# Kernel tuning notes

Hardware: AMD Instinct MI355X
Metric: run time of the kernel (lower is better)

## Reference

```python
import jax, jax.numpy as jnp
import numpy as np
import math

D, DF, H, L, V, T_MAX = 768, 3072, 12, 4, 32000, 2048
HD = D // H
B, T = 2, 2048


def setup_inputs() -> dict:
    key = jax.random.key(0)
    ks = jax.random.split(key, 20)
    s = 0.02
    inp = {
        'ids': jax.random.randint(ks[0], (B, T), 0, V),
        'te': jax.random.normal(ks[1], (V, D), jnp.float32) * s,  # tied with head
        'pe': jax.random.normal(ks[2], (T_MAX, D), jnp.float32) * s,
        'ln1_s': jnp.ones((L, D), jnp.float32),
        'ln1_b': jnp.zeros((L, D), jnp.float32),
        'qkv_w': jax.random.normal(ks[3], (L, D, 3 * H * HD), jnp.float32) * s,
        'qkv_b': jnp.zeros((L, 3 * H * HD), jnp.float32),
        'out_w': jax.random.normal(ks[4], (L, H * HD, D), jnp.float32) * s,
        'out_b': jnp.zeros((L, D), jnp.float32),
        'ln2_s': jnp.ones((L, D), jnp.float32),
        'ln2_b': jnp.zeros((L, D), jnp.float32),
        'up_w': jax.random.normal(ks[5], (L, D, DF), jnp.float32) * s,
        'up_b': jnp.zeros((L, DF), jnp.float32),
        'dn_w': jax.random.normal(ks[6], (L, DF, D), jnp.float32) * s,
        'dn_b': jnp.zeros((L, D), jnp.float32),
        'lnf_s': jnp.ones((D,), jnp.float32),
        'lnf_b': jnp.zeros((D,), jnp.float32),
    }
    return inp


def _layernorm(x, s, b, eps=1e-5):
    mu = jnp.mean(x, axis=-1, keepdims=True)
    var = jnp.mean(jnp.square(x - mu), axis=-1, keepdims=True)
    return (x - mu) * jax.lax.rsqrt(var + eps) * s + b


def reference(ids, te, pe, ln1_s, ln1_b, qkv_w, qkv_b, out_w, out_b,
              ln2_s, ln2_b, up_w, up_b, dn_w, dn_b, lnf_s, lnf_b):
    b, t = ids.shape
    x = te[ids] + pe[jnp.arange(t)][None, :, :]  # [b,t,d]
    causal = jnp.tril(jnp.ones((t, t), bool))[None, None]  # [1,1,t,t]
    neg = jnp.asarray(-jnp.inf, x.dtype)
    for i in range(L):
        h = _layernorm(x, ln1_s[i], ln1_b[i])
        qkv = (h @ qkv_w[i] + qkv_b[i]).reshape(b, t, 3, H, HD)
        q, k, v = [jnp.moveaxis(qkv[:, :, j], 1, 2) for j in range(3)]  # [b,h,t,hd]
        sc = jnp.einsum('bhqd,bhkd->bhqk', q, k) / math.sqrt(HD)
        sc = jnp.where(causal, sc, neg)
        a = jax.nn.softmax(sc, axis=-1)
        o = jnp.einsum('bhqk,bhkd->bhqd', a, v)
        o = jnp.moveaxis(o, 1, 2).reshape(b, t, H * HD)
        x = x + o @ out_w[i] + out_b[i]
        h = _layernorm(x, ln2_s[i], ln2_b[i])
        x = x + jax.nn.silu(h @ up_w[i] + up_b[i]) @ dn_w[i] + dn_b[i]
    logits = _layernorm(x, lnf_s, lnf_b) @ te.T  # tied head, no bias
    return logits
```

## Files before the change

### kernel.cpp

```cpp
#include <hip/hip_runtime.h>

typedef unsigned short u16;

#define TSEQ 2048
#define DMODEL 768
#define DFF 3072
#define NHEAD 12
#define HDIM 64
#define NLAYER 4
#define NVOCAB 32000
#define MROWS 4096

typedef __attribute__((ext_vector_type(8))) __bf16 bf16x8;
typedef __attribute__((ext_vector_type(4))) float f32x4;
typedef __attribute__((ext_vector_type(8))) unsigned short us8;

__device__ __forceinline__ float u2f(u16 u) {
  return __uint_as_float(((unsigned int)u) << 16);
}
__device__ __forceinline__ u16 f2bu(float f) {
  unsigned int u = __float_as_uint(f);
  u += 0x7fffu + ((u >> 16) & 1u);
  return (u16)(u >> 16);
}
__device__ __forceinline__ int probe_f32(const void* probe) {
  return ((const u16*)probe)[0] == 0 ? 1 : 0;
}
__device__ __forceinline__ float ldf(const void* p, size_t i, int f32) {
  return f32 ? ((const float*)p)[i] : u2f(((const u16*)p)[i]);
}
__device__ __forceinline__ void ld8(const void* p, size_t i, int f32, float* o) {
  if (f32) {
    const float* q = (const float*)p + i;
    float4 a = *(const float4*)q, b = *(const float4*)(q + 4);
    o[0]=a.x; o[1]=a.y; o[2]=a.z; o[3]=a.w; o[4]=b.x; o[5]=b.y; o[6]=b.z; o[7]=b.w;
  } else {
    const u16* q = (const u16*)p + i;
    ushort4 a = *(const ushort4*)q, b = *(const ushort4*)(q + 4);
    o[0]=u2f(a.x); o[1]=u2f(a.y); o[2]=u2f(a.z); o[3]=u2f(a.w);
    o[4]=u2f(b.x); o[5]=u2f(b.y); o[6]=u2f(b.z); o[7]=u2f(b.w);
  }
}
__device__ __forceinline__ us8 pack8(const float* f) {
  us8 r;
#pragma unroll
  for (int i = 0; i < 8; i++) r[i] = f2bu(f[i]);
  return r;
}
__device__ __forceinline__ void gld16(const u16* g, u16* l) {
  __builtin_amdgcn_global_load_lds(
      (const __attribute__((address_space(1))) void*)g,
      (__attribute__((address_space(3))) void*)l, 16, 0, 0);
}

__global__ __launch_bounds__(256) void embed_kernel(const int* __restrict__ ids,
    const void* __restrict__ te, const void* __restrict__ pe, float* __restrict__ x,
    const void* probe) {
  int f32 = probe_f32(probe);
  int m = blockIdx.x;
  int t = m & (TSEQ - 1);
  int id = ids[m];
  float* xr = x + (size_t)m * DMODEL;
  for (int d = threadIdx.x; d < DMODEL; d += 256)
    xr[d] = ldf(te, (size_t)id * DMODEL + d, f32) + ldf(pe, (size_t)t * DMODEL + d, f32);
}

__global__ __launch_bounds__(256) void ln_kernel(const float* __restrict__ x,
    const void* __restrict__ s, const void* __restrict__ b, long soff,
    u16* __restrict__ h, const void* probe) {
  int f32 = probe_f32(probe);
  int m = blockIdx.x;
  const float* xr = x + (size_t)m * DMODEL;
  float v[3];
  float lsum = 0.f, lsq = 0.f;
#pragma unroll
  for (int j = 0; j < 3; j++) {
    float t = xr[threadIdx.x + j * 256];
    v[j] = t; lsum += t; lsq += t * t;
  }
#pragma unroll
  for (int off = 32; off > 0; off >>= 1) {
    lsum += __shfl_down(lsum, off);
    lsq  += __shfl_down(lsq, off);
  }
  __shared__ float wsum[4], wsq[4];
  __shared__ float mu_s, rs_s;
  int wid = threadIdx.x >> 6, lane = threadIdx.x & 63;
  if (lane == 0) { wsum[wid] = lsum; wsq[wid] = lsq; }
  __syncthreads();
  if (threadIdx.x == 0) {
    float su = wsum[0] + wsum[1] + wsum[2] + wsum[3];
    float sq = wsq[0] + wsq[1] + wsq[2] + wsq[3];
    float mu = su * (1.f / DMODEL);
    float var = sq * (1.f / DMODEL) - mu * mu;
    mu_s = mu;
    rs_s = rsqrtf(var + 1e-5f);
  }
  __syncthreads();
  float mu = mu_s, rs = rs_s;
  u16* hr = h + (size_t)m * DMODEL;
#pragma unroll
  for (int j = 0; j < 3; j++) {
    int d = threadIdx.x + j * 256;
    hr[d] = f2bu((v[j] - mu) * rs * ldf(s, soff + d, f32) + ldf(b, soff + d, f32));
  }
}

__global__ __launch_bounds__(256) void wtrans_kernel(const void* __restrict__ W,
    u16* __restrict__ Wt, int K, int N, const void* probe) {
  const int f32 = probe_f32(probe);
  __shared__ u16 t[64][33];
  const size_t ls = (size_t)K * N;
  const size_t off = (size_t)blockIdx.z * ls;
  const int k0 = blockIdx.y << 6, n0 = blockIdx.x << 5;
  const int tid = threadIdx.x;
  const int tn = tid & 31, tk8 = tid >> 5;
#pragma unroll
  for (int p = 0; p < 8; p++) {
    int k = (p << 3) + tk8;
    t[k][tn] = f2bu(ldf(W, off + (size_t)(k0 + k) * N + n0 + tn, f32));
  }
  __syncthreads();
  const int kp = (tid & 31) << 1, nb = tid >> 5;
#pragma unroll
  for (int p = 0; p < 4; p++) {
    int n = (p << 3) + nb;
    ushort2 v; v.x = t[kp][n]; v.y = t[kp + 1][n];
    *(ushort2*)&Wt[off + (size_t)(n0 + n) * K + k0 + kp] = v;
  }
}

__global__ __launch_bounds__(256) void cvt_bf16_kernel(const void* __restrict__ src,
    u16* __restrict__ dst, size_t n, const void* probe) {
  const int f32 = probe_f32(probe);
  size_t i = ((size_t)blockIdx.x * 256 + threadIdx.x) * 8;
  if (i >= n) return;
  float v[8];
  ld8(src, i, f32, v);
  *(us8*)&dst[i] = pack8(v);
}

__global__ __launch_bounds__(256) void gemm_mfma(const u16* __restrict__ A,
    const u16* __restrict__ Wt, long woff, const void* __restrict__ bias, long boff,
    const float* resid, void* C, int N, int K, int mode, const void* probe) {
  const int f32 = probe_f32(probe);
  __shared__ __align__(16) u16 As[128 * 32];
  __shared__ __align__(16) u16 Bs[128 * 32];
  const int tid = threadIdx.x;
  const int m0 = blockIdx.y << 7, n0 = blockIdx.x << 7;
  const int lane = tid & 63;
  const int w = tid >> 6;
  const int wr = ((tid >> 7) & 1) << 6;
  const int wc = ((tid >> 6) & 1) << 6;
  const int fm = lane & 15;
  const int kl = lane >> 4;
  const int srow = (w << 4) + (lane >> 2);
  const int skc  = (lane & 3) << 3;

  f32x4 acc[4][4];
#pragma unroll
  for (int i = 0; i < 4; i++)
#pragma unroll
    for (int j = 0; j < 4; j++) acc[i][j] = (f32x4){0.f, 0.f, 0.f, 0.f};

  const u16* Ab = A + (size_t)(m0 + srow) * K + skc;
  const u16* Wb = Wt + (size_t)woff + (size_t)(n0 + srow) * K + skc;
  const size_t rstep = (size_t)64 * K;
  u16* lA0 = As + (w << 9);
  u16* lA1 = As + ((w + 4) << 9);
  u16* lB0 = Bs + (w << 9);
  u16* lB1 = Bs + ((w + 4) << 9);

  for (int k0 = 0; k0 < K; k0 += 32) {
    gld16(Ab + k0, lA0);
    gld16(Ab + rstep + k0, lA1);
    gld16(Wb + k0, lB0);
    gld16(Wb + rstep + k0, lB1);
    __syncthreads();
    bf16x8 af[4], bfr[4];
#pragma unroll
    for (int i = 0; i < 4; i++)
      af[i] = *reinterpret_cast<const bf16x8*>(&As[((wr + i * 16 + fm) << 5) + (kl << 3)]);
#pragma unroll
    for (int j = 0; j < 4; j++)
      bfr[j] = *reinterpret_cast<const bf16x8*>(&Bs[((wc + j * 16 + fm) << 5) + (kl << 3)]);
#pragma unroll
    for (int i = 0; i < 4; i++)
#pragma unroll
      for (int j = 0; j < 4; j++)
        acc[i][j] = __builtin_amdgcn_mfma_f32_16x16x32_bf16(af[i], bfr[j], acc[i][j], 0, 0, 0);
    __syncthreads();
  }

  const int rb = m0 + wr + (kl << 2);
  const int cb = n0 + wc + fm;
  float bv[4];
#pragma unroll
  for (int j = 0; j < 4; j++) bv[j] = ldf(bias, boff + cb + j * 16, f32);
#pragma unroll
  for (int i = 0; i < 4; i++) {
#pragma unroll
    for (int e = 0; e < 4; e++) {
      size_t roff = (size_t)(rb + i * 16 + e) * N;
#pragma unroll
      for (int j = 0; j < 4; j++) {
        float v = acc[i][j][e] + bv[j];
        if (mode == 1) {
          ((float*)C)[roff + cb + j * 16] = v + resid[roff + cb + j * 16];
        } else {
          if (mode == 2) v = v / (1.f + __expf(-v));
          ((u16*)C)[roff + cb + j * 16] = f2bu(v);
        }
      }
    }
  }
}

__global__ __launch_bounds__(256) void gemm_head_mfma(const u16* __restrict__ A,
    const u16* __restrict__ Wtb, void* __restrict__ C, const void* probe) {
  const int f32 = probe_f32(probe);
  __shared__ __align__(16) u16 As[128 * 32];
  __shared__ __align__(16) u16 Bs[128 * 32];
  const int tid = threadIdx.x;
  const int m0 = blockIdx.x << 7, n0 = blockIdx.y << 7;
  const int lane = tid & 63;
  const int w = tid >> 6;
  const int wr = ((tid >> 7) & 1) << 6;
  const int wc = ((tid >> 6) & 1) << 6;
  const int fm = lane & 15;
  const int kl = lane >> 4;
  const int srow = (w << 4) + (lane >> 2);
  const int skc  = (lane & 3) << 3;

  f32x4 acc[4][4];
#pragma unroll
  for (int i = 0; i < 4; i++)
#pragma unroll
    for (int j = 0; j < 4; j++) acc[i][j] = (f32x4){0.f, 0.f, 0.f, 0.f};

  const u16* Ab = A + (size_t)(m0 + srow) * DMODEL + skc;
  const u16* Wb = Wtb + (size_t)(n0 + srow) * DMODEL + skc;
  const size_t rstep = (size_t)64 * DMODEL;
  u16* lA0 = As + (w << 9);
  u16* lA1 = As + ((w + 4) << 9);
  u16* lB0 = Bs + (w << 9);
  u16* lB1 = Bs + ((w + 4) << 9);

  for (int k0 = 0; k0 < DMODEL; k0 += 32) {
    gld16(Ab + k0, lA0);
    gld16(Ab + rstep + k0, lA1);
    gld16(Wb + k0, lB0);
    gld16(Wb + rstep + k0, lB1);
    __syncthreads();
    bf16x8 af[4], bfr[4];
#pragma unroll
    for (int i = 0; i < 4; i++)
      af[i] = *reinterpret_cast<const bf16x8*>(&As[((wr + i * 16 + fm) << 5) + (kl << 3)]);
#pragma unroll
    for (int j = 0; j < 4; j++)
      bfr[j] = *reinterpret_cast<const bf16x8*>(&Bs[((wc + j * 16 + fm) << 5) + (kl << 3)]);
#pragma unroll
    for (int i = 0; i < 4; i++)
#pragma unroll
      for (int j = 0; j < 4; j++)
        acc[i][j] = __builtin_amdgcn_mfma_f32_16x16x32_bf16(af[i], bfr[j], acc[i][j], 0, 0, 0);
    __syncthreads();
  }

  const int rbase = m0 + wr + (kl << 2);
  const int cbase = n0 + wc + fm;
#pragma unroll
  for (int i = 0; i < 4; i++) {
#pragma unroll
    for (int j = 0; j < 4; j++) {
#pragma unroll
      for (int e = 0; e < 4; e++) {
        size_t off = (size_t)(rbase + i * 16 + e) * NVOCAB + cbase + j * 16;
        if (f32) ((float*)C)[off] = acc[i][j][e];
        else     ((u16*)C)[off]   = f2bu(acc[i][j][e]);
      }
    }
  }
}

__global__ __launch_bounds__(256) void attn_mfma(const u16* __restrict__ qkv,
                                                 u16* __restrict__ o) {
  const int qt = blockIdx.x, hh = blockIdx.y, bb = blockIdx.z;
  __shared__ __align__(16) u16 Ks[64][72];
  __shared__ __align__(16) u16 Vt[64][72];
  __shared__ __align__(16) u16 Ps[64][72];
  const int tid = threadIdx.x;
  const int w = tid >> 6, lane = tid & 63;
  const int fm = lane & 15, kl = lane >> 4;

  bf16x8 aq[2];
  {
    const u16* qrow = qkv + ((size_t)(bb * TSEQ + qt * 64 + w * 16 + fm)) * 2304 + hh * 64;
#pragma unroll
    for (int c = 0; c < 2; c++) {
      us8 u = *(const us8*)(qrow + c * 32 + kl * 8);
      aq[c] = *(bf16x8*)&u;
    }
  }

  float m_r[4], l_r[4];
#pragma unroll
  for (int e = 0; e < 4; e++) { m_r[e] = -3e38f; l_r[e] = 0.f; }
  f32x4 oacc[4];
#pragma unroll
  for (int j = 0; j < 4; j++) oacc[j] = (f32x4){0.f, 0.f, 0.f, 0.f};

  for (int kt = 0; kt <= qt; kt++) {
    const size_t kbase = ((size_t)(bb * TSEQ + kt * 64)) * 2304 + hh * 64;
#pragma unroll
    for (int it = 0; it < 2; it++) {
      int idx = tid + it * 256;
      int row = idx >> 3, cb = (idx & 7) << 3;
      *(us8*)&Ks[row][cb] = *(const us8*)(qkv + kbase + (size_t)row * 2304 + 768 + cb);
      int row2 = idx & 63, cb2 = (idx >> 6) << 3;
      us8 vv = *(const us8*)(qkv + kbase + (size_t)row2 * 2304 + 1536 + cb2);
#pragma unroll
      for (int e = 0; e < 8; e++) Vt[cb2 + e][row2] = vv[e];
    }
    __syncthreads();

    f32x4 sacc[4];
#pragma unroll
    for (int j = 0; j < 4; j++) sacc[j] = (f32x4){0.f, 0.f, 0.f, 0.f};
#pragma unroll
    for (int ck = 0; ck < 2; ck++) {
      bf16x8 kb[4];
#pragma unroll
      for (int j = 0; j < 4; j++)
        kb[j] = *reinterpret_cast<const bf16x8*>(&Ks[j * 16 + fm][ck * 32 + (kl << 3)]);
#pragma unroll
      for (int j = 0; j < 4; j++)
        sacc[j] = __builtin_amdgcn_mfma_f32_16x16x32_bf16(aq[ck], kb[j], sacc[j], 0, 0, 0);
    }
#pragma unroll
    for (int j = 0; j < 4; j++)
#pragma unroll
      for (int e = 0; e < 4; e++) sacc[j][e] *= 0.125f;
    if (kt == qt) {
      const int qrow0 = w * 16 + (kl << 2);
#pragma unroll
      for (int j = 0; j < 4; j++)
#pragma unroll
        for (int e = 0; e < 4; e++)
          if (j * 16 + fm > qrow0 + e) sacc[j][e] = -3e38f;
    }
    float pmax[4];
#pragma unroll
    for (int e = 0; e < 4; e++) {
      pmax[e] = fmaxf(fmaxf(sacc[0][e], sacc[1][e]), fmaxf(sacc[2][e], sacc[3][e]));
    }
#pragma unroll
    for (int msk = 1; msk < 16; msk <<= 1)
#pragma unroll
      for (int e = 0; e < 4; e++) pmax[e] = fmaxf(pmax[e], __shfl_xor(pmax[e], msk));
    float al[4];
#pragma unroll
    for (int e = 0; e < 4; e++) {
      float nm = fmaxf(m_r[e], pmax[e]);
      al[e] = __expf(m_r[e] - nm);
      m_r[e] = nm;
    }
    float psum[4] = {0.f, 0.f, 0.f, 0.f};
#pragma unroll
    for (int j = 0; j < 4; j++)
#pragma unroll
      for (int e = 0; e < 4; e++) {
        float p = __expf(sacc[j][e] - m_r[e]);
        sacc[j][e] = p;
        psum[e] += p;
      }
#pragma unroll
    for (int j = 0; j < 4; j++)
#pragma unroll
      for (int e = 0; e < 4; e++)
        Ps[w * 16 + (kl << 2) + e][j * 16 + fm] = f2bu(sacc[j][e]);
#pragma unroll
    for (int msk = 1; msk < 16; msk <<= 1)
#pragma unroll
      for (int e = 0; e < 4; e++) psum[e] += __shfl_xor(psum[e], msk);
#pragma unroll
    for (int e = 0; e < 4; e++) l_r[e] = l_r[e] * al[e] + psum[e];
#pragma unroll
    for (int j = 0; j < 4; j++)
#pragma unroll
      for (int e = 0; e < 4; e++) oacc[j][e] *= al[e];
#pragma unroll
    for (int ck = 0; ck < 2; ck++) {
      bf16x8 pa = *reinterpret_cast<const bf16x8*>(&Ps[w * 16 + fm][ck * 32 + (kl << 3)]);
      bf16x8 vb[4];
#pragma unroll
      for (int j = 0; j < 4; j++)
        vb[j] = *reinterpret_cast<const bf16x8*>(&Vt[j * 16 + fm][ck * 32 + (kl << 3)]);
#pragma unroll
      for (int j = 0; j < 4; j++)
        oacc[j] = __builtin_amdgcn_mfma_f32_16x16x32_bf16(pa, vb[j], oacc[j], 0, 0, 0);
    }
    __syncthreads();
  }

  float linv[4];
#pragma unroll
  for (int e = 0; e < 4; e++) linv[e] = 1.f / l_r[e];
#pragma unroll
  for (int e = 0; e < 4; e++) {
    size_t ob = ((size_t)(bb * TSEQ + qt * 64 + w * 16 + (kl << 2) + e)) * DMODEL + hh * 64 + fm;
#pragma unroll
    for (int j = 0; j < 4; j++) o[ob + j * 16] = f2bu(oacc[j][e] * linv[e]);
  }
}

extern "C" void kernel_launch(void* const* d_in, const int* in_sizes, int n_in,
                              void* d_out, int out_size, void* d_ws, size_t ws_size,
                              hipStream_t stream) {
  const int* ids = (const int*)d_in[0];
  const void* te    = d_in[1];
  const void* pe    = d_in[2];
  const void* ln1_s = d_in[3];
  const void* ln1_b = d_in[4];
  const void* qkv_w = d_in[5];
  const void* qkv_b = d_in[6];
  const void* out_w = d_in[7];
  const void* out_b = d_in[8];
  const void* ln2_s = d_in[9];
  const void* ln2_b = d_in[10];
  const void* up_w  = d_in[11];
  const void* up_b  = d_in[12];
  const void* dn_w  = d_in[13];
  const void* dn_b  = d_in[14];
  const void* lnf_s = d_in[15];
  const void* lnf_b = d_in[16];
  const void* probe = ln1_s;

  float* x  = (float*)d_ws;
  u16* h    = (u16*)(x + (size_t)MROWS * DMODEL);
  u16* ob   = h + (size_t)MROWS * DMODEL;
  u16* qu   = ob + (size_t)MROWS * DMODEL;
  u16* wt   = qu + (size_t)MROWS * DFF;
  const size_t qkv_t_sz = (size_t)2304 * 768;
  const size_t out_t_sz = (size_t)768 * 768;
  const size_t up_t_sz  = (size_t)3072 * 768;
  const size_t dn_t_sz  = (size_t)768 * 3072;
  u16* qkv_t = wt;
  u16* out_t = qkv_t + NLAYER * qkv_t_sz;
  u16* up_t  = out_t + NLAYER * out_t_sz;
  u16* dn_t  = up_t  + NLAYER * up_t_sz;
  u16* tebf  = dn_t + NLAYER * dn_t_sz;
  const size_t te_sz = (size_t)NVOCAB * DMODEL;

  embed_kernel<<<MROWS, 256, 0, stream>>>(ids, te, pe, x, probe);

  wtrans_kernel<<<dim3(2304/32, 768/64, NLAYER), 256, 0, stream>>>(qkv_w, qkv_t, 768, 2304, probe);
  wtrans_kernel<<<dim3(768/32,  768/64, NLAYER), 256, 0, stream>>>(out_w, out_t, 768, 768, probe);
  wtrans_kernel<<<dim3(3072/32, 768/64, NLAYER), 256, 0, stream>>>(up_w,  up_t,  768, 3072, probe);
  wtrans_kernel<<<dim3(768/32, 3072/64, NLAYER), 256, 0, stream>>>(dn_w,  dn_t,  3072, 768, probe);
  cvt_bf16_kernel<<<(int)((te_sz / 8 + 255) / 256), 256, 0, stream>>>(te, tebf, te_sz, probe);

  for (int l = 0; l < NLAYER; l++) {
    long lD = (long)l * DMODEL;
    ln_kernel<<<MROWS, 256, 0, stream>>>(x, ln1_s, ln1_b, lD, h, probe);
    gemm_mfma<<<dim3(18, 32), 256, 0, stream>>>(h, qkv_t, (long)l * qkv_t_sz,
        qkv_b, (long)l * 2304, nullptr, qu, 2304, DMODEL, 0, probe);
    attn_mfma<<<dim3(32, 12, 2), 256, 0, stream>>>(qu, ob);
    gemm_mfma<<<dim3(6, 32), 256, 0, stream>>>(ob, out_t, (long)l * out_t_sz,
        out_b, lD, x, x, DMODEL, DMODEL, 1, probe);
    ln_kernel<<<MROWS, 256, 0, stream>>>(x, ln2_s, ln2_b, lD, h, probe);
    gemm_mfma<<<dim3(24, 32), 256, 0, stream>>>(h, up_t, (long)l * up_t_sz,
        up_b, (long)l * DFF, nullptr, qu, DFF, DMODEL, 2, probe);
    gemm_mfma<<<dim3(6, 32), 256, 0, stream>>>(qu, dn_t, (long)l * dn_t_sz,
        dn_b, lD, x, x, DMODEL, DFF, 1, probe);
  }
  ln_kernel<<<MROWS, 256, 0, stream>>>(x, lnf_s, lnf_b, 0, h, probe);
  gemm_head_mfma<<<dim3(32, 250), 256, 0, stream>>>(h, tebf, d_out, probe);
}
```

Before: 2.302 ms.

## Enlarge attention query tile to 128 rows with register-prefetched K/V and reversed scheduling

The attention kernel now processes 128 query rows per block, with each wave handling two 16-row groups, so every K/V tile loaded into shared memory is reused across twice as many queries. The next K/V tile is prefetched into registers while the current tile is computed. Blocks are launched in reverse order so the heaviest causal tiles start first. In exchange, register pressure rises, the grid shrinks to half as many blocks, and waves whose rows are fully masked sit idle on the last tile.

Measured after the change: 2.377 ms. 1.03x slower.

```diff
diff --git a/kernel.cpp b/kernel.cpp
--- a/kernel.cpp
+++ b/kernel.cpp
@@ -285,132 +285,182 @@
 
 __global__ __launch_bounds__(256) void attn_mfma(const u16* __restrict__ qkv,
                                                  u16* __restrict__ o) {
-  const int qt = blockIdx.x, hh = blockIdx.y, bb = blockIdx.z;
+  const int qb = gridDim.x - 1 - blockIdx.x;
+  const int hh = blockIdx.y, bb = blockIdx.z;
   __shared__ __align__(16) u16 Ks[64][72];
   __shared__ __align__(16) u16 Vt[64][72];
-  __shared__ __align__(16) u16 Ps[64][72];
+  __shared__ __align__(16) u16 Ps[128][72];
   const int tid = threadIdx.x;
   const int w = tid >> 6, lane = tid & 63;
   const int fm = lane & 15, kl = lane >> 4;
 
-  bf16x8 aq[2];
-  {
-    const u16* qrow = qkv + ((size_t)(bb * TSEQ + qt * 64 + w * 16 + fm)) * 2304 + hh * 64;
+  const int krow0 = tid >> 3, kcb0 = (tid & 7) << 3;
+  const int krow1 = (tid + 256) >> 3, kcb1 = ((tid + 256) & 7) << 3;
+  const int vrow0 = tid & 63, vcb0 = (tid >> 6) << 3;
+  const int vcb1 = vcb0 + 32;
+
+  bf16x8 aq[2][2];
+#pragma unroll
+  for (int g = 0; g < 2; g++) {
+    const u16* qrow = qkv + ((size_t)(bb * TSEQ + qb * 128 + w * 32 + g * 16 + fm)) * 2304 + hh * 64;
 #pragma unroll
     for (int c = 0; c < 2; c++) {
       us8 u = *(const us8*)(qrow + c * 32 + kl * 8);
-      aq[c] = *(bf16x8*)&u;
-    }
-  }
-
-  float m_r[4], l_r[4];
-#pragma unroll
-  for (int e = 0; e < 4; e++) { m_r[e] = -3e38f; l_r[e] = 0.f; }
-  f32x4 oacc[4];
-#pragma unroll
-  for (int j = 0; j < 4; j++) oacc[j] = (f32x4){0.f, 0.f, 0.f, 0.f};
-
-  for (int kt = 0; kt <= qt; kt++) {
-    const size_t kbase = ((size_t)(bb * TSEQ + kt * 64)) * 2304 + hh * 64;
-#pragma unroll
-    for (int it = 0; it < 2; it++) {
-      int idx = tid + it * 256;
-      int row = idx >> 3, cb = (idx & 7) << 3;
-      *(us8*)&Ks[row][cb] = *(const us8*)(qkv + kbase + (size_t)row * 2304 + 768 + cb);
-      int row2 = idx & 63, cb2 = (idx >> 6) << 3;
-      us8 vv = *(const us8*)(qkv + kbase + (size_t)row2 * 2304 + 1536 + cb2);
-#pragma unroll
-      for (int e = 0; e < 8; e++) Vt[cb2 + e][row2] = vv[e];
+      aq[g][c] = *(bf16x8*)&u;
+    }
+  }
+
+  float m_r[2][4], l_r[2][4];
+#pragma unroll
+  for (int g = 0; g < 2; g++)
+#pragma unroll
+    for (int e = 0; e < 4; e++) { m_r[g][e] = -3e38f; l_r[g][e] = 0.f; }
+  f32x4 oacc[2][4];
+#pragma unroll
+  for (int g = 0; g < 2; g++)
+#pragma unroll
+    for (int j = 0; j < 4; j++) oacc[g][j] = (f32x4){0.f, 0.f, 0.f, 0.f};
+
+  const int ktop  = 2 * qb + 1;
+  const int kmaxw = 2 * qb + (w >> 1);
+
+  {
+    const size_t kb0 = ((size_t)(bb * TSEQ)) * 2304 + hh * 64;
+    *(us8*)&Ks[krow0][kcb0] = *(const us8*)(qkv + kb0 + (size_t)krow0 * 2304 + 768 + kcb0);
+    *(us8*)&Ks[krow1][kcb1] = *(const us8*)(qkv + kb0 + (size_t)krow1 * 2304 + 768 + kcb1);
+    us8 v0 = *(const us8*)(qkv + kb0 + (size_t)vrow0 * 2304 + 1536 + vcb0);
+    us8 v1 = *(const us8*)(qkv + kb0 + (size_t)vrow0 * 2304 + 1536 + vcb1);
+#pragma unroll
+    for (int e = 0; e < 8; e++) { Vt[vcb0 + e][vrow0] = v0[e]; Vt[vcb1 + e][vrow0] = v1[e]; }
+  }
+  __syncthreads();
+
+  for (int kt = 0; kt <= ktop; kt++) {
+    const int active = (kt <= kmaxw);
+    f32x4 sacc[2][4];
+#pragma unroll
+    for (int g = 0; g < 2; g++)
+#pragma unroll
+      for (int j = 0; j < 4; j++) sacc[g][j] = (f32x4){0.f, 0.f, 0.f, 0.f};
+    if (active) {
+#pragma unroll
+      for (int ck = 0; ck < 2; ck++) {
+        bf16x8 kb[4];
+#pragma unroll
+        for (int j = 0; j < 4; j++)
+          kb[j] = *reinterpret_cast<const bf16x8*>(&Ks[j * 16 + fm][ck * 32 + (kl << 3)]);
+#pragma unroll
+        for (int g = 0; g < 2; g++)
+#pragma unroll
+          for (int j = 0; j < 4; j++)
+            sacc[g][j] = __builtin_amdgcn_mfma_f32_16x16x32_bf16(aq[g][ck], kb[j], sacc[g][j], 0, 0, 0);
+      }
+    }
+    us8 kpre0, kpre1, vpre0, vpre1;
+    const int nkt = kt + 1;
+    if (nkt <= ktop) {
+      const size_t kbn = ((size_t)(bb * TSEQ + nkt * 64)) * 2304 + hh * 64;
+      kpre0 = *(const us8*)(qkv + kbn + (size_t)krow0 * 2304 + 768 + kcb0);
+      kpre1 = *(const us8*)(qkv + kbn + (size_t)krow1 * 2304 + 768 + kcb1);
+      vpre0 = *(const us8*)(qkv + kbn + (size_t)vrow0 * 2304 + 1536 + vcb0);
+      vpre1 = *(const us8*)(qkv + kbn + (size_t)vrow0 * 2304 + 1536 + vcb1);
+    }
+    if (active) {
+#pragma unroll
+      for (int g = 0; g < 2; g++)
+#pragma unroll
+        for (int j = 0; j < 4; j++)
+#pragma unroll
+          for (int e = 0; e < 4; e++) sacc[g][j][e] *= 0.125f;
+      if (kt == kmaxw) {
+#pragma unroll
+        for (int g = 0; g < 2; g++) {
+          const int qg = qb * 128 + w * 32 + g * 16 + (kl << 2);
+#pragma unroll
+          for (int j = 0; j < 4; j++)
+#pragma unroll
+            for (int e = 0; e < 4; e++)
+              if (kt * 64 + j * 16 + fm > qg + e) sacc[g][j][e] = -3e38f;
+        }
+      }
+#pragma unroll
+      for (int g = 0; g < 2; g++) {
+        float pmax[4];
+#pragma unroll
+        for (int e = 0; e < 4; e++)
+          pmax[e] = fmaxf(fmaxf(sacc[g][0][e], sacc[g][1][e]), fmaxf(sacc[g][2][e], sacc[g][3][e]));
+#pragma unroll
+        for (int msk = 1; msk < 16; msk <<= 1)
+#pragma unroll
+          for (int e = 0; e < 4; e++) pmax[e] = fmaxf(pmax[e], __shfl_xor(pmax[e], msk));
+        float al[4];
+#pragma unroll
+        for (int e = 0; e < 4; e++) {
+          float nm = fmaxf(m_r[g][e], pmax[e]);
+          al[e] = __expf(m_r[g][e] - nm);
+          m_r[g][e] = nm;
+        }
+        float psum[4] = {0.f, 0.f, 0.f, 0.f};
+#pragma unroll
+        for (int j = 0; j < 4; j++)
+#pragma unroll
+          for (int e = 0; e < 4; e++) {
+            float p = __expf(sacc[g][j][e] - m_r[g][e]);
+            sacc[g][j][e] = p;
+            psum[e] += p;
+          }
+#pragma unroll
+        for (int j = 0; j < 4; j++)
+#pragma unroll
+          for (int e = 0; e < 4; e++)
+            Ps[w * 32 + g * 16 + (kl << 2) + e][j * 16 + fm] = f2bu(sacc[g][j][e]);
+#pragma unroll
+        for (int msk = 1; msk < 16; msk <<= 1)
+#pragma unroll
+          for (int e = 0; e < 4; e++) psum[e] += __shfl_xor(psum[e], msk);
+#pragma unroll
+        for (int e = 0; e < 4; e++) l_r[g][e] = l_r[g][e] * al[e] + psum[e];
+#pragma unroll
+        for (int j = 0; j < 4; j++)
+#pragma unroll
+          for (int e = 0; e < 4; e++) oacc[g][j][e] *= al[e];
+      }
+#pragma unroll
+      for (int ck = 0; ck < 2; ck++) {
+        bf16x8 vb[4];
+#pragma unroll
+        for (int j = 0; j < 4; j++)
+          vb[j] = *reinterpret_cast<const bf16x8*>(&Vt[j * 16 + fm][ck * 32 + (kl << 3)]);
+#pragma unroll
+        for (int g = 0; g < 2; g++) {
+          bf16x8 pa = *reinterpret_cast<const bf16x8*>(&Ps[w * 32 + g * 16 + fm][ck * 32 + (kl << 3)]);
+#pragma unroll
+          for (int j = 0; j < 4; j++)
+            oacc[g][j] = __builtin_amdgcn_mfma_f32_16x16x32_bf16(pa, vb[j], oacc[g][j], 0, 0, 0);
+        }
+      }
     }
     __syncthreads();
-
-    f32x4 sacc[4];
-#pragma unroll
-    for (int j = 0; j < 4; j++) sacc[j] = (f32x4){0.f, 0.f, 0.f, 0.f};
-#pragma unroll
-    for (int ck = 0; ck < 2; ck++) {
-      bf16x8 kb[4];
-#pragma unroll
-      for (int j = 0; j < 4; j++)
-        kb[j] = *reinterpret_cast<const bf16x8*>(&Ks[j * 16 + fm][ck * 32 + (kl << 3)]);
-#pragma unroll
-      for (int j = 0; j < 4; j++)
-        sacc[j] = __builtin_amdgcn_mfma_f32_16x16x32_bf16(aq[ck], kb[j], sacc[j], 0, 0, 0);
-    }
-#pragma unroll
-    for (int j = 0; j < 4; j++)
-#pragma unroll
-      for (int e = 0; e < 4; e++) sacc[j][e] *= 0.125f;
-    if (kt == qt) {
-      const int qrow0 = w * 16 + (kl << 2);
-#pragma unroll
-      for (int j = 0; j < 4; j++)
-#pragma unroll
-        for (int e = 0; e < 4; e++)
-          if (j * 16 + fm > qrow0 + e) sacc[j][e] = -3e38f;
-    }
-    float pmax[4];
+    if (nkt <= ktop) {
+      *(us8*)&Ks[krow0][kcb0] = kpre0;
+      *(us8*)&Ks[krow1][kcb1] = kpre1;
+#pragma unroll
+      for (int e = 0; e < 8; e++) { Vt[vcb0 + e][vrow0] = vpre0[e]; Vt[vcb1 + e][vrow0] = vpre1[e]; }
+    }
+    __syncthreads();
+  }
+
+#pragma unroll
+  for (int g = 0; g < 2; g++) {
+    float linv[4];
+#pragma unroll
+    for (int e = 0; e < 4; e++) linv[e] = 1.f / l_r[g][e];
 #pragma unroll
     for (int e = 0; e < 4; e++) {
-      pmax[e] = fmaxf(fmaxf(sacc[0][e], sacc[1][e]), fmaxf(sacc[2][e], sacc[3][e]));
-    }
-#pragma unroll
-    for (int msk = 1; msk < 16; msk <<= 1)
-#pragma unroll
-      for (int e = 0; e < 4; e++) pmax[e] = fmaxf(pmax[e], __shfl_xor(pmax[e], msk));
-    float al[4];
-#pragma unroll
-    for (int e = 0; e < 4; e++) {
-      float nm = fmaxf(m_r[e], pmax[e]);
-      al[e] = __expf(m_r[e] - nm);
-      m_r[e] = nm;
-    }
-    float psum[4] = {0.f, 0.f, 0.f, 0.f};
-#pragma unroll
-    for (int j = 0; j < 4; j++)
-#pragma unroll
-      for (int e = 0; e < 4; e++) {
-        float p = __expf(sacc[j][e] - m_r[e]);
-        sacc[j][e] = p;
-        psum[e] += p;
-      }
-#pragma unroll
-    for (int j = 0; j < 4; j++)
-#pragma unroll
-      for (int e = 0; e < 4; e++)
-        Ps[w * 16 + (kl << 2) + e][j * 16 + fm] = f2bu(sacc[j][e]);
-#pragma unroll
-    for (int msk = 1; msk < 16; msk <<= 1)
-#pragma unroll
-      for (int e = 0; e < 4; e++) psum[e] += __shfl_xor(psum[e], msk);
-#pragma unroll
-    for (int e = 0; e < 4; e++) l_r[e] = l_r[e] * al[e] + psum[e];
-#pragma unroll
-    for (int j = 0; j < 4; j++)
-#pragma unroll
-      for (int e = 0; e < 4; e++) oacc[j][e] *= al[e];
-#pragma unroll
-    for (int ck = 0; ck < 2; ck++) {
-      bf16x8 pa = *reinterpret_cast<const bf16x8*>(&Ps[w * 16 + fm][ck * 32 + (kl << 3)]);
-      bf16x8 vb[4];
-#pragma unroll
-      for (int j = 0; j < 4; j++)
-        vb[j] = *reinterpret_cast<const bf16x8*>(&Vt[j * 16 + fm][ck * 32 + (kl << 3)]);
-#pragma unroll
-      for (int j = 0; j < 4; j++)
-        oacc[j] = __builtin_amdgcn_mfma_f32_16x16x32_bf16(pa, vb[j], oacc[j], 0, 0, 0);
-    }
-    __syncthreads();
-  }
-
-  float linv[4];
-#pragma unroll
-  for (int e = 0; e < 4; e++) linv[e] = 1.f / l_r[e];
-#pragma unroll
-  for (int e = 0; e < 4; e++) {
-    size_t ob = ((size_t)(bb * TSEQ + qt * 64 + w * 16 + (kl << 2) + e)) * DMODEL + hh * 64 + fm;
-#pragma unroll
-    for (int j = 0; j < 4; j++) o[ob + j * 16] = f2bu(oacc[j][e] * linv[e]);
+      size_t ob = ((size_t)(bb * TSEQ + qb * 128 + w * 32 + g * 16 + (kl << 2) + e)) * DMODEL + hh * 64 + fm;
+#pragma unroll
+      for (int j = 0; j < 4; j++) o[ob + j * 16] = f2bu(oacc[g][j][e] * linv[e]);
+    }
   }
 }
 
@@ -465,7 +515,7 @@
     ln_kernel<<<MROWS, 256, 0, stream>>>(x, ln1_s, ln1_b, lD, h, probe);
     gemm_mfma<<<dim3(18, 32), 256, 0, stream>>>(h, qkv_t, (long)l * qkv_t_sz,
         qkv_b, (long)l * 2304, nullptr, qu, 2304, DMODEL, 0, probe);
-    attn_mfma<<<dim3(32, 12, 2), 256, 0, stream>>>(qu, ob);
+    attn_mfma<<<dim3(16, 12, 2), 256, 0, stream>>>(qu, ob);
     gemm_mfma<<<dim3(6, 32), 256, 0, stream>>>(ob, out_t, (long)l * out_t_sz,
         out_b, lD, x, x, DMODEL, DMODEL, 1, probe);
     ln_kernel<<<MROWS, 256, 0, stream>>>(x, ln2_s, ln2_b, lD, h, probe);
```

## Enlarge attention query tile to 128 with register-prefetched K/V and reversed block order

Applied to the files above, without the earlier changes.

The attention kernel now uses 512 threads per block covering 128 query rows, so each K/V tile loaded into shared memory serves twice as many queries. The next K/V tile is fetched into registers while the current tile is being computed, then written to LDS after a barrier, which overlaps global load latency with MFMA and softmax work. Blocks are launched in reverse order so the longest causal rows start first, improving load balance. The cost is wasted iterations for the lower-half waves on the last tile, larger blocks, and an extra barrier per iteration.

After: 2.357 ms. 1.02x slower.

```diff
diff --git a/kernel.cpp b/kernel.cpp
--- a/kernel.cpp
+++ b/kernel.cpp
@@ -283,19 +283,23 @@
   }
 }
 
-__global__ __launch_bounds__(256) void attn_mfma(const u16* __restrict__ qkv,
+__global__ __launch_bounds__(512) void attn_mfma(const u16* __restrict__ qkv,
                                                  u16* __restrict__ o) {
-  const int qt = blockIdx.x, hh = blockIdx.y, bb = blockIdx.z;
+  const int qb = gridDim.x - 1 - blockIdx.x;
+  const int hh = blockIdx.y, bb = blockIdx.z;
   __shared__ __align__(16) u16 Ks[64][72];
   __shared__ __align__(16) u16 Vt[64][72];
-  __shared__ __align__(16) u16 Ps[64][72];
+  __shared__ __align__(16) u16 Ps[128][72];
   const int tid = threadIdx.x;
   const int w = tid >> 6, lane = tid & 63;
   const int fm = lane & 15, kl = lane >> 4;
 
+  const int krow = tid >> 3, kcb = (tid & 7) << 3;
+  const int vrow = tid & 63, vcb = (tid >> 6) << 3;
+
   bf16x8 aq[2];
   {
-    const u16* qrow = qkv + ((size_t)(bb * TSEQ + qt * 64 + w * 16 + fm)) * 2304 + hh * 64;
+    const u16* qrow = qkv + ((size_t)(bb * TSEQ + qb * 128 + w * 16 + fm)) * 2304 + hh * 64;
 #pragma unroll
     for (int c = 0; c < 2; c++) {
       us8 u = *(const us8*)(qrow + c * 32 + kl * 8);
@@ -310,95 +314,111 @@
 #pragma unroll
   for (int j = 0; j < 4; j++) oacc[j] = (f32x4){0.f, 0.f, 0.f, 0.f};
 
-  for (int kt = 0; kt <= qt; kt++) {
-    const size_t kbase = ((size_t)(bb * TSEQ + kt * 64)) * 2304 + hh * 64;
-#pragma unroll
-    for (int it = 0; it < 2; it++) {
-      int idx = tid + it * 256;
-      int row = idx >> 3, cb = (idx & 7) << 3;
-      *(us8*)&Ks[row][cb] = *(const us8*)(qkv + kbase + (size_t)row * 2304 + 768 + cb);
-      int row2 = idx & 63, cb2 = (idx >> 6) << 3;
-      us8 vv = *(const us8*)(qkv + kbase + (size_t)row2 * 2304 + 1536 + cb2);
-#pragma unroll
-      for (int e = 0; e < 8; e++) Vt[cb2 + e][row2] = vv[e];
-    }
-    __syncthreads();
-
+  const int ktop  = 2 * qb + 1;
+  const int kmaxw = 2 * qb + (w >> 2);
+
+  {
+    const size_t kb0 = ((size_t)(bb * TSEQ)) * 2304 + hh * 64;
+    *(us8*)&Ks[krow][kcb] = *(const us8*)(qkv + kb0 + (size_t)krow * 2304 + 768 + kcb);
+    us8 v0 = *(const us8*)(qkv + kb0 + (size_t)vrow * 2304 + 1536 + vcb);
+#pragma unroll
+    for (int e = 0; e < 8; e++) Vt[vcb + e][vrow] = v0[e];
+  }
+  __syncthreads();
+
+  for (int kt = 0; kt <= ktop; kt++) {
+    const int active = (kt <= kmaxw);
     f32x4 sacc[4];
 #pragma unroll
     for (int j = 0; j < 4; j++) sacc[j] = (f32x4){0.f, 0.f, 0.f, 0.f};
-#pragma unroll
-    for (int ck = 0; ck < 2; ck++) {
-      bf16x8 kb[4];
-#pragma unroll
-      for (int j = 0; j < 4; j++)
-        kb[j] = *reinterpret_cast<const bf16x8*>(&Ks[j * 16 + fm][ck * 32 + (kl << 3)]);
-#pragma unroll
-      for (int j = 0; j < 4; j++)
-        sacc[j] = __builtin_amdgcn_mfma_f32_16x16x32_bf16(aq[ck], kb[j], sacc[j], 0, 0, 0);
-    }
-#pragma unroll
-    for (int j = 0; j < 4; j++)
-#pragma unroll
-      for (int e = 0; e < 4; e++) sacc[j][e] *= 0.125f;
-    if (kt == qt) {
-      const int qrow0 = w * 16 + (kl << 2);
+    if (active) {
+#pragma unroll
+      for (int ck = 0; ck < 2; ck++) {
+        bf16x8 kb[4];
+#pragma unroll
+        for (int j = 0; j < 4; j++)
+          kb[j] = *reinterpret_cast<const bf16x8*>(&Ks[j * 16 + fm][ck * 32 + (kl << 3)]);
+#pragma unroll
+        for (int j = 0; j < 4; j++)
+          sacc[j] = __builtin_amdgcn_mfma_f32_16x16x32_bf16(aq[ck], kb[j], sacc[j], 0, 0, 0);
+      }
+    }
+    us8 kpre, vpre;
+    const int nkt = kt + 1;
+    if (nkt <= ktop) {
+      const size_t kbn = ((size_t)(bb * TSEQ + nkt * 64)) * 2304 + hh * 64;
+      kpre = *(const us8*)(qkv + kbn + (size_t)krow * 2304 + 768 + kcb);
+      vpre = *(const us8*)(qkv + kbn + (size_t)vrow * 2304 + 1536 + vcb);
+    }
+    if (active) {
+#pragma unroll
+      for (int j = 0; j < 4; j++)
+#pragma unroll
+        for (int e = 0; e < 4; e++) sacc[j][e] *= 0.125f;
+      if (kt == kmaxw) {
+        const int qg = qb * 128 + w * 16 + (kl << 2);
+#pragma unroll
+        for (int j = 0; j < 4; j++)
+#pragma unroll
+          for (int e = 0; e < 4; e++)
+            if (kt * 64 + j * 16 + fm > qg + e) sacc[j][e] = -3e38f;
+      }
+      float pmax[4];
+#pragma unroll
+      for (int e = 0; e < 4; e++)
+        pmax[e] = fmaxf(fmaxf(sacc[0][e], sacc[1][e]), fmaxf(sacc[2][e], sacc[3][e]));
+#pragma unroll
+      for (int msk = 1; msk < 16; msk <<= 1)
+#pragma unroll
+        for (int e = 0; e < 4; e++) pmax[e] = fmaxf(pmax[e], __shfl_xor(pmax[e], msk));
+      float al[4];
+#pragma unroll
+      for (int e = 0; e < 4; e++) {
+        float nm = fmaxf(m_r[e], pmax[e]);
+        al[e] = __expf(m_r[e] - nm);
+        m_r[e] = nm;
+      }
+      float psum[4] = {0.f, 0.f, 0.f, 0.f};
+#pragma unroll
+      for (int j = 0; j < 4; j++)
+#pragma unroll
+        for (int e = 0; e < 4; e++) {
+          float p = __expf(sacc[j][e] - m_r[e]);
+          sacc[j][e] = p;
+          psum[e] += p;
+        }
 #pragma unroll
       for (int j = 0; j < 4; j++)
 #pragma unroll
         for (int e = 0; e < 4; e++)
-          if (j * 16 + fm > qrow0 + e) sacc[j][e] = -3e38f;
-    }
-    float pmax[4];
-#pragma unroll
-    for (int e = 0; e < 4; e++) {
-      pmax[e] = fmaxf(fmaxf(sacc[0][e], sacc[1][e]), fmaxf(sacc[2][e], sacc[3][e]));
-    }
-#pragma unroll
-    for (int msk = 1; msk < 16; msk <<= 1)
-#pragma unroll
-      for (int e = 0; e < 4; e++) pmax[e] = fmaxf(pmax[e], __shfl_xor(pmax[e], msk));
-    float al[4];
-#pragma unroll
-    for (int e = 0; e < 4; e++) {
-      float nm = fmaxf(m_r[e], pmax[e]);
-      al[e] = __expf(m_r[e] - nm);
-      m_r[e] = nm;
-    }
-    float psum[4] = {0.f, 0.f, 0.f, 0.f};
-#pragma unroll
-    for (int j = 0; j < 4; j++)
-#pragma unroll
-      for (int e = 0; e < 4; e++) {
-        float p = __expf(sacc[j][e] - m_r[e]);
-        sacc[j][e] = p;
-        psum[e] += p;
-      }
-#pragma unroll
-    for (int j = 0; j < 4; j++)
-#pragma unroll
-      for (int e = 0; e < 4; e++)
-        Ps[w * 16 + (kl << 2) + e][j * 16 + fm] = f2bu(sacc[j][e]);
-#pragma unroll
-    for (int msk = 1; msk < 16; msk <<= 1)
-#pragma unroll
-      for (int e = 0; e < 4; e++) psum[e] += __shfl_xor(psum[e], msk);
-#pragma unroll
-    for (int e = 0; e < 4; e++) l_r[e] = l_r[e] * al[e] + psum[e];
-#pragma unroll
-    for (int j = 0; j < 4; j++)
-#pragma unroll
-      for (int e = 0; e < 4; e++) oacc[j][e] *= al[e];
-#pragma unroll
-    for (int ck = 0; ck < 2; ck++) {
-      bf16x8 pa = *reinterpret_cast<const bf16x8*>(&Ps[w * 16 + fm][ck * 32 + (kl << 3)]);
-      bf16x8 vb[4];
-#pragma unroll
-      for (int j = 0; j < 4; j++)
-        vb[j] = *reinterpret_cast<const bf16x8*>(&Vt[j * 16 + fm][ck * 32 + (kl << 3)]);
-#pragma unroll
-      for (int j = 0; j < 4; j++)
-        oacc[j] = __builtin_amdgcn_mfma_f32_16x16x32_bf16(pa, vb[j], oacc[j], 0, 0, 0);
+          Ps[w * 16 + (kl << 2) + e][j * 16 + fm] = f2bu(sacc[j][e]);
+#pragma unroll
+      for (int msk = 1; msk < 16; msk <<= 1)
+#pragma unroll
+        for (int e = 0; e < 4; e++) psum[e] += __shfl_xor(psum[e], msk);
+#pragma unroll
+      for (int e = 0; e < 4; e++) l_r[e] = l_r[e] * al[e] + psum[e];
+#pragma unroll
+      for (int j = 0; j < 4; j++)
+#pragma unroll
+        for (int e = 0; e < 4; e++) oacc[j][e] *= al[e];
+#pragma unroll
+      for (int ck = 0; ck < 2; ck++) {
+        bf16x8 pa = *reinterpret_cast<const bf16x8*>(&Ps[w * 16 + fm][ck * 32 + (kl << 3)]);
+        bf16x8 vb[4];
+#pragma unroll
+        for (int j = 0; j < 4; j++)
+          vb[j] = *reinterpret_cast<const bf16x8*>(&Vt[j * 16 + fm][ck * 32 + (kl << 3)]);
+#pragma unroll
+        for (int j = 0; j < 4; j++)
+          oacc[j] = __builtin_amdgcn_mfma_f32_16x16x32_bf16(pa, vb[j], oacc[j], 0, 0, 0);
+      }
+    }
+    __syncthreads();
+    if (nkt <= ktop) {
+      *(us8*)&Ks[krow][kcb] = kpre;
+#pragma unroll
+      for (int e = 0; e < 8; e++) Vt[vcb + e][vrow] = vpre[e];
     }
     __syncthreads();
   }
@@ -408,7 +428,7 @@
   for (int e = 0; e < 4; e++) linv[e] = 1.f / l_r[e];
 #pragma unroll
   for (int e = 0; e < 4; e++) {
-    size_t ob = ((size_t)(bb * TSEQ + qt * 64 + w * 16 + (kl << 2) + e)) * DMODEL + hh * 64 + fm;
+    size_t ob = ((size_t)(bb * TSEQ + qb * 128 + w * 16 + (kl << 2) + e)) * DMODEL + hh * 64 + fm;
 #pragma unroll
     for (int j = 0; j < 4; j++) o[ob + j * 16] = f2bu(oacc[j][e] * linv[e]);
   }
@@ -465,7 +485,7 @@
     ln_kernel<<<MROWS, 256, 0, stream>>>(x, ln1_s, ln1_b, lD, h, probe);
     gemm_mfma<<<dim3(18, 32), 256, 0, stream>>>(h, qkv_t, (long)l * qkv_t_sz,
         qkv_b, (long)l * 2304, nullptr, qu, 2304, DMODEL, 0, probe);
-    attn_mfma<<<dim3(32, 12, 2), 256, 0, stream>>>(qu, ob);
+    attn_mfma<<<dim3(16, 12, 2), 512, 0, stream>>>(qu, ob);
     gemm_mfma<<<dim3(6, 32), 256, 0, stream>>>(ob, out_t, (long)l * out_t_sz,
         out_b, lD, x, x, DMODEL, DMODEL, 1, probe);
     ln_kernel<<<MROWS, 256, 0, stream>>>(x, ln2_s, ln2_b, lD, h, probe);
```

## Prefetch K/V into registers in attention, reverse tile order, widen head GEMM K-tile

Applied to the files above, without the earlier changes.

The attention kernel now starts the global loads for the next K/V tile into registers while the current tile is being computed, then writes them to shared memory after a barrier. This overlaps load latency with compute at the cost of more registers and an extra barrier per iteration. Query blocks are also scheduled in reverse, so the longest causal rows launch first and load balancing improves. Separately, the tied-head GEMM now uses a K-tile of 64 instead of 32, which halves the number of barriers and loop iterations but doubles the shared memory per block.

New measurement: 2.271 ms. About the same (-1.4%).

```diff
diff --git a/kernel.cpp b/kernel.cpp
--- a/kernel.cpp
+++ b/kernel.cpp
@@ -219,8 +219,8 @@
 __global__ __launch_bounds__(256) void gemm_head_mfma(const u16* __restrict__ A,
     const u16* __restrict__ Wtb, void* __restrict__ C, const void* probe) {
   const int f32 = probe_f32(probe);
-  __shared__ __align__(16) u16 As[128 * 32];
-  __shared__ __align__(16) u16 Bs[128 * 32];
+  __shared__ __align__(16) u16 As[128 * 64];
+  __shared__ __align__(16) u16 Bs[128 * 64];
   const int tid = threadIdx.x;
   const int m0 = blockIdx.x << 7, n0 = blockIdx.y << 7;
   const int lane = tid & 63;
@@ -229,8 +229,8 @@
   const int wc = ((tid >> 6) & 1) << 6;
   const int fm = lane & 15;
   const int kl = lane >> 4;
-  const int srow = (w << 4) + (lane >> 2);
-  const int skc  = (lane & 3) << 3;
+  const int srow = (w << 5) + (lane >> 3);
+  const int skc  = (lane & 7) << 3;
 
   f32x4 acc[4][4];
 #pragma unroll
@@ -240,30 +240,31 @@
 
   const u16* Ab = A + (size_t)(m0 + srow) * DMODEL + skc;
   const u16* Wb = Wtb + (size_t)(n0 + srow) * DMODEL + skc;
-  const size_t rstep = (size_t)64 * DMODEL;
-  u16* lA0 = As + (w << 9);
-  u16* lA1 = As + ((w + 4) << 9);
-  u16* lB0 = Bs + (w << 9);
-  u16* lB1 = Bs + ((w + 4) << 9);
-
-  for (int k0 = 0; k0 < DMODEL; k0 += 32) {
-    gld16(Ab + k0, lA0);
-    gld16(Ab + rstep + k0, lA1);
-    gld16(Wb + k0, lB0);
-    gld16(Wb + rstep + k0, lB1);
-    __syncthreads();
-    bf16x8 af[4], bfr[4];
-#pragma unroll
-    for (int i = 0; i < 4; i++)
-      af[i] = *reinterpret_cast<const bf16x8*>(&As[((wr + i * 16 + fm) << 5) + (kl << 3)]);
-#pragma unroll
-    for (int j = 0; j < 4; j++)
-      bfr[j] = *reinterpret_cast<const bf16x8*>(&Bs[((wc + j * 16 + fm) << 5) + (kl << 3)]);
-#pragma unroll
-    for (int i = 0; i < 4; i++)
-#pragma unroll
-      for (int j = 0; j < 4; j++)
-        acc[i][j] = __builtin_amdgcn_mfma_f32_16x16x32_bf16(af[i], bfr[j], acc[i][j], 0, 0, 0);
+  u16* lA = As + (w << 11);
+  u16* lB = Bs + (w << 11);
+
+  for (int k0 = 0; k0 < DMODEL; k0 += 64) {
+#pragma unroll
+    for (int i = 0; i < 4; i++) {
+      gld16(Ab + (size_t)(8 * i) * DMODEL + k0, lA + (i << 9));
+      gld16(Wb + (size_t)(8 * i) * DMODEL + k0, lB + (i << 9));
+    }
+    __syncthreads();
+#pragma unroll
+    for (int kh = 0; kh < 2; kh++) {
+      bf16x8 af[4], bfr[4];
+#pragma unroll
+      for (int i = 0; i < 4; i++)
+        af[i] = *reinterpret_cast<const bf16x8*>(&As[((wr + i * 16 + fm) << 6) + (kh << 5) + (kl << 3)]);
+#pragma unroll
+      for (int j = 0; j < 4; j++)
+        bfr[j] = *reinterpret_cast<const bf16x8*>(&Bs[((wc + j * 16 + fm) << 6) + (kh << 5) + (kl << 3)]);
+#pragma unroll
+      for (int i = 0; i < 4; i++)
+#pragma unroll
+        for (int j = 0; j < 4; j++)
+          acc[i][j] = __builtin_amdgcn_mfma_f32_16x16x32_bf16(af[i], bfr[j], acc[i][j], 0, 0, 0);
+    }
     __syncthreads();
   }
 
@@ -285,7 +286,8 @@
 
 __global__ __launch_bounds__(256) void attn_mfma(const u16* __restrict__ qkv,
                                                  u16* __restrict__ o) {
-  const int qt = blockIdx.x, hh = blockIdx.y, bb = blockIdx.z;
+  const int qb = gridDim.x - 1 - blockIdx.x;
+  const int hh = blockIdx.y, bb = blockIdx.z;
   __shared__ __align__(16) u16 Ks[64][72];
   __shared__ __align__(16) u16 Vt[64][72];
   __shared__ __align__(16) u16 Ps[64][72];
@@ -293,9 +295,14 @@
   const int w = tid >> 6, lane = tid & 63;
   const int fm = lane & 15, kl = lane >> 4;
 
+  const int krow0 = tid >> 3, kcb0 = (tid & 7) << 3;
+  const int krow1 = (tid + 256) >> 3, kcb1 = ((tid + 256) & 7) << 3;
+  const int vrow = tid & 63, vcb0 = (tid >> 6) << 3;
+  const int vcb1 = vcb0 + 32;
+
   bf16x8 aq[2];
   {
-    const u16* qrow = qkv + ((size_t)(bb * TSEQ + qt * 64 + w * 16 + fm)) * 2304 + hh * 64;
+    const u16* qrow = qkv + ((size_t)(bb * TSEQ + qb * 64 + w * 16 + fm)) * 2304 + hh * 64;
 #pragma unroll
     for (int c = 0; c < 2; c++) {
       us8 u = *(const us8*)(qrow + c * 32 + kl * 8);
@@ -310,20 +317,18 @@
 #pragma unroll
   for (int j = 0; j < 4; j++) oacc[j] = (f32x4){0.f, 0.f, 0.f, 0.f};
 
-  for (int kt = 0; kt <= qt; kt++) {
-    const size_t kbase = ((size_t)(bb * TSEQ + kt * 64)) * 2304 + hh * 64;
-#pragma unroll
-    for (int it = 0; it < 2; it++) {
-      int idx = tid + it * 256;
-      int row = idx >> 3, cb = (idx & 7) << 3;
-      *(us8*)&Ks[row][cb] = *(const us8*)(qkv + kbase + (size_t)row * 2304 + 768 + cb);
-      int row2 = idx & 63, cb2 = (idx >> 6) << 3;
-      us8 vv = *(const us8*)(qkv + kbase + (size_t)row2 * 2304 + 1536 + cb2);
-#pragma unroll
-      for (int e = 0; e < 8; e++) Vt[cb2 + e][row2] = vv[e];
-    }
-    __syncthreads();
-
+  {
+    const size_t kb0 = ((size_t)(bb * TSEQ)) * 2304 + hh * 64;
+    *(us8*)&Ks[krow0][kcb0] = *(const us8*)(qkv + kb0 + (size_t)krow0 * 2304 + 768 + kcb0);
+    *(us8*)&Ks[krow1][kcb1] = *(const us8*)(qkv + kb0 + (size_t)krow1 * 2304 + 768 + kcb1);
+    us8 v0 = *(const us8*)(qkv + kb0 + (size_t)vrow * 2304 + 1536 + vcb0);
+    us8 v1 = *(const us8*)(qkv + kb0 + (size_t)vrow * 2304 + 1536 + vcb1);
+#pragma unroll
+    for (int e = 0; e < 8; e++) { Vt[vcb0 + e][vrow] = v0[e]; Vt[vcb1 + e][vrow] = v1[e]; }
+  }
+  __syncthreads();
+
+  for (int kt = 0; kt <= qb; kt++) {
     f32x4 sacc[4];
 #pragma unroll
     for (int j = 0; j < 4; j++) sacc[j] = (f32x4){0.f, 0.f, 0.f, 0.f};
@@ -337,11 +342,20 @@
       for (int j = 0; j < 4; j++)
         sacc[j] = __builtin_amdgcn_mfma_f32_16x16x32_bf16(aq[ck], kb[j], sacc[j], 0, 0, 0);
     }
+    us8 kpre0, kpre1, vpre0, vpre1;
+    const int nkt = kt + 1;
+    if (nkt <= qb) {
+      const size_t kbn = ((size_t)(bb * TSEQ + nkt * 64)) * 2304 + hh * 64;
+      kpre0 = *(const us8*)(qkv + kbn + (size_t)krow0 * 2304 + 768 + kcb0);
+      kpre1 = *(const us8*)(qkv + kbn + (size_t)krow1 * 2304 + 768 + kcb1);
+      vpre0 = *(const us8*)(qkv + kbn + (size_t)vrow * 2304 + 1536 + vcb0);
+      vpre1 = *(const us8*)(qkv + kbn + (size_t)vrow * 2304 + 1536 + vcb1);
+    }
 #pragma unroll
     for (int j = 0; j < 4; j++)
 #pragma unroll
       for (int e = 0; e < 4; e++) sacc[j][e] *= 0.125f;
-    if (kt == qt) {
+    if (kt == qb) {
       const int qrow0 = w * 16 + (kl << 2);
 #pragma unroll
       for (int j = 0; j < 4; j++)
@@ -351,9 +365,8 @@
     }
     float pmax[4];
 #pragma unroll
-    for (int e = 0; e < 4; e++) {
+    for (int e = 0; e < 4; e++)
       pmax[e] = fmaxf(fmaxf(sacc[0][e], sacc[1][e]), fmaxf(sacc[2][e], sacc[3][e]));
-    }
 #pragma unroll
     for (int msk = 1; msk < 16; msk <<= 1)
 #pragma unroll
@@ -401,6 +414,13 @@
         oacc[j] = __builtin_amdgcn_mfma_f32_16x16x32_bf16(pa, vb[j], oacc[j], 0, 0, 0);
     }
     __syncthreads();
+    if (nkt <= qb) {
+      *(us8*)&Ks[krow0][kcb0] = kpre0;
+      *(us8*)&Ks[krow1][kcb1] = kpre1;
+#pragma unroll
+      for (int e = 0; e < 8; e++) { Vt[vcb0 + e][vrow] = vpre0[e]; Vt[vcb1 + e][vrow] = vpre1[e]; }
+    }
+    __syncthreads();
   }
 
   float linv[4];
@@ -408,7 +428,7 @@
   for (int e = 0; e < 4; e++) linv[e] = 1.f / l_r[e];
 #pragma unroll
   for (int e = 0; e < 4; e++) {
-    size_t ob = ((size_t)(bb * TSEQ + qt * 64 + w * 16 + (kl << 2) + e)) * DMODEL + hh * 64 + fm;
+    size_t ob = ((size_t)(bb * TSEQ + qb * 64 + w * 16 + (kl << 2) + e)) * DMODEL + hh * 64 + fm;
 #pragma unroll
     for (int j = 0; j < 4; j++) o[ob + j * 16] = f2bu(oacc[j][e] * linv[e]);
   }
```
